# Optimization experiments

Hardware: AMD Instinct MI355X
Metric: run time of the kernel (lower is better)

Reference implementation:

```python
import jax, jax.numpy as jnp
import numpy as np

QMIN, QMAX = -128, 127  # signed int8 range


def setup_inputs() -> dict:
    key = jax.random.key(0)
    k_x, k_w, k_b = jax.random.split(key, 3)
    N, C_in, H, W = 32, 128, 56, 56
    C_out, kH, kW = 256, 3, 3
    # int8-valued tensors carried as int32 (jax-friendly); values in [-128, 127]
    x = jax.random.randint(k_x, (N, C_in, H, W), 0, 256, dtype=jnp.int32) - 128
    weight = jax.random.randint(k_w, (C_out, C_in, kH, kW), 0, 256, dtype=jnp.int32) - 128
    # int32 bias, already quantized with scale s_in * s_w
    bias = jax.random.randint(k_b, (C_out,), -(2 ** 14), 2 ** 14, dtype=jnp.int32)
    return {
        "x": x,
        "weight": weight,
        "bias": bias,
        "input_scale": jnp.float32(0.02),
        "weight_scale": jnp.float32(0.005),
        "output_scale": jnp.float32(0.05),
        "input_zero_point": jnp.int32(-5),
        "output_zero_point": jnp.int32(3),
    }


def reference(x, weight, bias, input_scale, weight_scale, output_scale,
              input_zero_point, output_zero_point):
    # Dequant-style integer conv: shift input by its zero point (weights are
    # symmetric, zero point 0), accumulate in fp32 (stands in for int32 acc).
    x_f = (x - input_zero_point).astype(jnp.float32)
    w_f = weight.astype(jnp.float32)
    acc = jax.lax.conv_general_dilated(
        x_f, w_f,
        window_strides=(1, 1),
        padding=((1, 1), (1, 1)),
        dimension_numbers=("NCHW", "OIHW", "NCHW"),
    )
    acc = acc + bias.astype(jnp.float32)[None, :, None, None]
    # Requantize: scale fusion + output zero point, round, clamp to int8.
    requant_scale = input_scale * weight_scale / output_scale
    y = acc * requant_scale + output_zero_point.astype(jnp.float32)
    y_q = jnp.clip(jnp.round(y), QMIN, QMAX).astype(jnp.int8)
    return y_q
```

## Files before the change

### kernel.cpp

```cpp
#include <hip/hip_runtime.h>
#include <stdint.h>


#define NB 32
#define CI 128
#define HH 56
#define WW 56
#define CO 256
#define SPA (HH * WW)
#define HP 58
#define WP 64
#define XP2_BYTES (NB * HP * WP * CI)
#define BP_BYTES (9 * 2 * 4 * CO * 16)
#define ABUF (6 * 8192)

typedef int v4i __attribute__((ext_vector_type(4)));

__global__ __launch_bounds__(256) void prep_kernel(
    const int* __restrict__ x, const int* __restrict__ wgt,
    const int* __restrict__ bias, const int* __restrict__ zpi,
    int8_t* __restrict__ xp2, int8_t* __restrict__ bp, int* __restrict__ BG)
{
    __shared__ int sm[1824];
    const int tid = threadIdx.x, bid = blockIdx.x;
    const int zp = *zpi;
    const int zp4 = (zp & 255) * 0x01010101;

    if (bid < HH * NB) {
        const int n = bid / HH, h = bid % HH;
        #pragma unroll
        for (int it = 0; it < 7; ++it) {
            int j = tid + it * 256;
            int ci = j / 14, w4 = j - ci * 14;
            const v4i v = *(const v4i*)(x + ((n * CI + ci) * HH + h) * WW + w4 * 4);
            sm[w4 * 130 + ci] = (v.x & 255) | ((v.y & 255) << 8) |
                                ((v.z & 255) << 16) | (v.w << 24);
        }
        __syncthreads();
        int* od = (int*)xp2 + (n * HP + h + 1) * (WP * CI / 4);
        #pragma unroll
        for (int it = 0; it < 8; ++it) {
            int j = tid + it * 256;
            int widx = j >> 5, ci4 = j & 31;
            int val = zp4;
            if (widx >= 1 && widx <= WW) {
                int w = widx - 1;
                int base = (w >> 2) * 130 + ci4 * 4;
                int sh = (w & 3) * 8;
                val = ((sm[base] >> sh) & 0xff) | (((sm[base+1] >> sh) & 0xff) << 8) |
                      (((sm[base+2] >> sh) & 0xff) << 16) | ((sm[base+3] >> sh) << 24);
            }
            od[j ^ ((widx & 7) << 2)] = val;
        }
    } else if (bid < HH * NB + 2 * NB) {
        const int z = bid - HH * NB;
        const int n = z >> 1, hidx = (z & 1) ? (HP - 1) : 0;
        int* od = (int*)xp2 + (n * HP + hidx) * (WP * CI / 4);
        #pragma unroll
        for (int it = 0; it < 8; ++it) od[tid + it * 256] = zp4;
    } else {
        const int co = bid - (HH * NB + 2 * NB);
        for (int j = tid; j < 1152; j += 256) sm[j] = wgt[co * 1152 + j];
        __syncthreads();
        for (int j = tid; j < 288; j += 256) {
            int j4 = j & 3, q = (j >> 2) & 3, c64 = (j >> 4) & 1, t = j >> 5;
            int ci = c64 * 64 + q * 16 + j4 * 4;
            int b0 = sm[(ci + 0) * 9 + t] & 255, b1 = sm[(ci + 1) * 9 + t] & 255;
            int b2 = sm[(ci + 2) * 9 + t] & 255, b3 = sm[(ci + 3) * 9 + t];
            ((int*)bp)[((t * 2 + c64) * 4 + q) * 1024 + co * 4 + j4] =
                b0 | (b1 << 8) | (b2 << 16) | (b3 << 24);
        }
        if (tid < 9) {
            int s = 0;
            for (int ci = 0; ci < CI; ++ci) s += sm[ci * 9 + tid];
            sm[1152 + tid] = s;
        }
        __syncthreads();
        if (tid == 0) {
            int s9 = 0;
            for (int t = 0; t < 9; ++t) s9 += sm[1152 + t];
            BG[co] = bias[co] - zp * s9;
        }
    }
}

__global__ __launch_bounds__(256, 1) void qconv_mfma(
    const int8_t* __restrict__ xp2, const int8_t* __restrict__ bp,
    const int* __restrict__ BG,
    const float* __restrict__ si, const float* __restrict__ sw,
    const float* __restrict__ so, const int* __restrict__ zpo,
    int* __restrict__ out)
{
    const int tid  = threadIdx.x, lane = tid & 63, wid = tid >> 6;
    const int quad = lane >> 4, lo16 = lane & 15;
    const int bid  = blockIdx.x;
    const int x    = bid & 7, r = bid >> 3;
    const int n    = x * 4 + (r & 3);
    const int co64 = (r >> 2) & 3;
    const int p    = r >> 4;
    const int mh   = wid >> 1, ch = wid & 1;
    const int cw   = co64 * 64 + ch * 32;

    __shared__ __attribute__((aligned(16))) int8_t Asm[2][ABUF];

    const int8_t* src0 = xp2 + (((size_t)n * HP + 4 * p) << 13);
    #pragma unroll
    for (int k = 0; k < 12; ++k) {
        const int u = wid + 4 * k;
        __builtin_amdgcn_global_load_lds(
            (const __attribute__((address_space(1))) void*)(src0 + (u << 10) + lane * 16),
            (__attribute__((address_space(3))) void*)(&Asm[0][u << 10]), 16, 0, 0);
    }

    v4i breg[9][2][2];
    #pragma unroll
    for (int t = 0; t < 9; ++t)
        #pragma unroll
        for (int c = 0; c < 2; ++c)
            #pragma unroll
            for (int ct = 0; ct < 2; ++ct)
                breg[t][c][ct] = *(const v4i*)(bp + (((t * 2 + c) * 4 + quad) << 12) +
                                               (cw + ct * 16 + lo16) * 16);

    int bgv[2];
    #pragma unroll
    for (int ct = 0; ct < 2; ++ct) bgv[ct] = BG[cw + ct * 16 + lo16];
    const float rs = (*si) * (*sw) / (*so);
    const float zo = (float)(*zpo);

    int rowoff[7], colp[7][3];
    #pragma unroll
    for (int mt = 0; mt < 7; ++mt) {
        const int ml = mh * 112 + mt * 16 + lo16;
        const int srow = ml / 56, scol = ml - srow * 56;
        rowoff[mt] = srow * 8192;
        #pragma unroll
        for (int dc = 0; dc < 3; ++dc) {
            const int c2 = scol + dc;
            colp[mt][dc] = (c2 * 128 + quad * 16) ^ ((c2 & 7) << 4);
        }
    }

    __syncthreads();

    #pragma unroll 1
    for (int t7 = 0; t7 < 7; ++t7) {
        const int s = p + 2 * t7;
        const int8_t* curA = Asm[t7 & 1];

        if (t7 < 6) {
            const int8_t* srcn = xp2 + (((size_t)n * HP + 4 * (s + 2)) << 13);
            int8_t* dst = (int8_t*)Asm[(t7 & 1) ^ 1];
            #pragma unroll
            for (int k = 0; k < 12; ++k) {
                const int u = wid + 4 * k;
                __builtin_amdgcn_global_load_lds(
                    (const __attribute__((address_space(1))) void*)(srcn + (u << 10) + lane * 16),
                    (__attribute__((address_space(3))) void*)(dst + (u << 10)), 16, 0, 0);
            }
        }
        __builtin_amdgcn_sched_barrier(0);

        v4i acc[7][2];
        #pragma unroll
        for (int mt = 0; mt < 7; ++mt)
            #pragma unroll
            for (int ct = 0; ct < 2; ++ct) acc[mt][ct] = (v4i){0, 0, 0, 0};

        #pragma unroll
        for (int tp = 0; tp < 9; ++tp) {
            const int dr = tp / 3, dc = tp % 3;
            #pragma unroll
            for (int mt = 0; mt < 7; ++mt) {
                const int off = rowoff[mt] + dr * 8192 + colp[mt][dc];
                v4i a0 = *(const v4i*)(curA + off);
                v4i a1 = *(const v4i*)(curA + (off ^ 64));
                acc[mt][0] = __builtin_amdgcn_mfma_i32_16x16x64_i8(a0, breg[tp][0][0], acc[mt][0], 0, 0, 0);
                acc[mt][1] = __builtin_amdgcn_mfma_i32_16x16x64_i8(a0, breg[tp][0][1], acc[mt][1], 0, 0, 0);
                acc[mt][0] = __builtin_amdgcn_mfma_i32_16x16x64_i8(a1, breg[tp][1][0], acc[mt][0], 0, 0, 0);
                acc[mt][1] = __builtin_amdgcn_mfma_i32_16x16x64_i8(a1, breg[tp][1][1], acc[mt][1], 0, 0, 0);
            }
        }

        const int m0 = s * 224 + mh * 112;
        #pragma unroll
        for (int mt = 0; mt < 7; ++mt) {
            #pragma unroll
            for (int ct = 0; ct < 2; ++ct) {
                v4i vv;
                #pragma unroll
                for (int i = 0; i < 4; ++i) {
                    float yv = rintf((float)(acc[mt][ct][i] + bgv[ct]) * rs + zo);
                    yv = fminf(fmaxf(yv, -128.f), 127.f);
                    vv[i] = (int)yv;
                }
                *(v4i*)(out + (n * CO + cw + ct * 16 + lo16) * SPA +
                        m0 + mt * 16 + quad * 4) = vv;
            }
        }

        if (t7 < 6) {
            __builtin_amdgcn_sched_barrier(0);
            asm volatile("s_waitcnt vmcnt(14)" ::: "memory");
            __builtin_amdgcn_s_barrier();
            __builtin_amdgcn_sched_barrier(0);
        }
    }
}

extern "C" void kernel_launch(void* const* d_in, const int* in_sizes, int n_in,
                              void* d_out, int out_size, void* d_ws, size_t ws_size,
                              hipStream_t stream) {
    const int*   x    = (const int*)d_in[0];
    const int*   wgt  = (const int*)d_in[1];
    const int*   bias = (const int*)d_in[2];
    const float* si   = (const float*)d_in[3];
    const float* sw   = (const float*)d_in[4];
    const float* so   = (const float*)d_in[5];
    const int*   zpi  = (const int*)d_in[6];
    const int*   zpo  = (const int*)d_in[7];
    int* out = (int*)d_out;

    int8_t* xp2 = (int8_t*)d_ws;
    int8_t* bp  = xp2 + XP2_BYTES;
    int*    bg  = (int*)(bp + BP_BYTES);

    prep_kernel<<<HH * NB + 2 * NB + CO, 256, 0, stream>>>(x, wgt, bias, zpi, xp2, bp, bg);
    qconv_mfma<<<256, 256, 0, stream>>>(xp2, bp, bg, si, sw, so, zpo, out);
}
```

Baseline: 187.4 us.

## Shrink conv tile to two output rows per step and double grid

```diff
diff --git a/kernel.cpp b/kernel.cpp
--- a/kernel.cpp
+++ b/kernel.cpp
@@ -12,7 +12,7 @@
 #define WP 64
 #define XP2_BYTES (NB * HP * WP * CI)
 #define BP_BYTES (9 * 2 * 4 * CO * 16)
-#define ABUF (6 * 8192)
+#define ABUF (4 * 8192)
 
 typedef int v4i __attribute__((ext_vector_type(4)));
 
@@ -84,7 +84,7 @@
     }
 }
 
-__global__ __launch_bounds__(256, 1) void qconv_mfma(
+__global__ __launch_bounds__(256, 2) void qconv_mfma(
     const int8_t* __restrict__ xp2, const int8_t* __restrict__ bp,
     const int* __restrict__ BG,
     const float* __restrict__ si, const float* __restrict__ sw,
@@ -97,41 +97,36 @@
     const int x    = bid & 7, r = bid >> 3;
     const int n    = x * 4 + (r & 3);
     const int co64 = (r >> 2) & 3;
-    const int p    = r >> 4;
-    const int mh   = wid >> 1, ch = wid & 1;
-    const int cw   = co64 * 64 + ch * 32;
+    const int g    = r >> 4;
+    const int cw   = co64 * 64 + wid * 16;
 
     __shared__ __attribute__((aligned(16))) int8_t Asm[2][ABUF];
 
-    const int8_t* src0 = xp2 + (((size_t)n * HP + 4 * p) << 13);
+    const int8_t* src0 = xp2 + (((size_t)n * HP + 2 * g) << 13);
     #pragma unroll
-    for (int k = 0; k < 12; ++k) {
+    for (int k = 0; k < 8; ++k) {
         const int u = wid + 4 * k;
         __builtin_amdgcn_global_load_lds(
             (const __attribute__((address_space(1))) void*)(src0 + (u << 10) + lane * 16),
             (__attribute__((address_space(3))) void*)(&Asm[0][u << 10]), 16, 0, 0);
     }
 
-    v4i breg[9][2][2];
+    v4i breg[9][2];
     #pragma unroll
     for (int t = 0; t < 9; ++t)
         #pragma unroll
         for (int c = 0; c < 2; ++c)
-            #pragma unroll
-            for (int ct = 0; ct < 2; ++ct)
-                breg[t][c][ct] = *(const v4i*)(bp + (((t * 2 + c) * 4 + quad) << 12) +
-                                               (cw + ct * 16 + lo16) * 16);
-
-    int bgv[2];
-    #pragma unroll
-    for (int ct = 0; ct < 2; ++ct) bgv[ct] = BG[cw + ct * 16 + lo16];
+            breg[t][c] = *(const v4i*)(bp + (((t * 2 + c) * 4 + quad) << 12) +
+                                       (cw + lo16) * 16);
+
+    const int bg0 = BG[cw + lo16];
     const float rs = (*si) * (*sw) / (*so);
     const float zo = (float)(*zpo);
 
     int rowoff[7], colp[7][3];
     #pragma unroll
     for (int mt = 0; mt < 7; ++mt) {
-        const int ml = mh * 112 + mt * 16 + lo16;
+        const int ml = mt * 16 + lo16;
         const int srow = ml / 56, scol = ml - srow * 56;
         rowoff[mt] = srow * 8192;
         #pragma unroll
@@ -141,18 +136,20 @@
         }
     }
 
+    int* optr = out + ((size_t)n * CO + cw + lo16) * SPA + quad * 4;
+
     __syncthreads();
 
     #pragma unroll 1
     for (int t7 = 0; t7 < 7; ++t7) {
-        const int s = p + 2 * t7;
+        const int s = g + 4 * t7;
         const int8_t* curA = Asm[t7 & 1];
 
         if (t7 < 6) {
-            const int8_t* srcn = xp2 + (((size_t)n * HP + 4 * (s + 2)) << 13);
+            const int8_t* srcn = xp2 + (((size_t)n * HP + 2 * (s + 4)) << 13);
             int8_t* dst = (int8_t*)Asm[(t7 & 1) ^ 1];
             #pragma unroll
-            for (int k = 0; k < 12; ++k) {
+            for (int k = 0; k < 8; ++k) {
                 const int u = wid + 4 * k;
                 __builtin_amdgcn_global_load_lds(
                     (const __attribute__((address_space(1))) void*)(srcn + (u << 10) + lane * 16),
@@ -161,11 +158,9 @@
         }
         __builtin_amdgcn_sched_barrier(0);
 
-        v4i acc[7][2];
-        #pragma unroll
-        for (int mt = 0; mt < 7; ++mt)
-            #pragma unroll
-            for (int ct = 0; ct < 2; ++ct) acc[mt][ct] = (v4i){0, 0, 0, 0};
+        v4i acc[7];
+        #pragma unroll
+        for (int mt = 0; mt < 7; ++mt) acc[mt] = (v4i){0, 0, 0, 0};
 
         #pragma unroll
         for (int tp = 0; tp < 9; ++tp) {
@@ -175,33 +170,27 @@
                 const int off = rowoff[mt] + dr * 8192 + colp[mt][dc];
                 v4i a0 = *(const v4i*)(curA + off);
                 v4i a1 = *(const v4i*)(curA + (off ^ 64));
-                acc[mt][0] = __builtin_amdgcn_mfma_i32_16x16x64_i8(a0, breg[tp][0][0], acc[mt][0], 0, 0, 0);
-                acc[mt][1] = __builtin_amdgcn_mfma_i32_16x16x64_i8(a0, breg[tp][0][1], acc[mt][1], 0, 0, 0);
-                acc[mt][0] = __builtin_amdgcn_mfma_i32_16x16x64_i8(a1, breg[tp][1][0], acc[mt][0], 0, 0, 0);
-                acc[mt][1] = __builtin_amdgcn_mfma_i32_16x16x64_i8(a1, breg[tp][1][1], acc[mt][1], 0, 0, 0);
-            }
-        }
-
-        const int m0 = s * 224 + mh * 112;
+                acc[mt] = __builtin_amdgcn_mfma_i32_16x16x64_i8(a0, breg[tp][0], acc[mt], 0, 0, 0);
+                acc[mt] = __builtin_amdgcn_mfma_i32_16x16x64_i8(a1, breg[tp][1], acc[mt], 0, 0, 0);
+            }
+        }
+
+        const int m0 = s * 112;
         #pragma unroll
         for (int mt = 0; mt < 7; ++mt) {
+            v4i vv;
             #pragma unroll
-            for (int ct = 0; ct < 2; ++ct) {
-                v4i vv;
-                #pragma unroll
-                for (int i = 0; i < 4; ++i) {
-                    float yv = rintf((float)(acc[mt][ct][i] + bgv[ct]) * rs + zo);
-                    yv = fminf(fmaxf(yv, -128.f), 127.f);
-                    vv[i] = (int)yv;
-                }
-                *(v4i*)(out + (n * CO + cw + ct * 16 + lo16) * SPA +
-                        m0 + mt * 16 + quad * 4) = vv;
-            }
+            for (int i = 0; i < 4; ++i) {
+                float yv = rintf((float)(acc[mt][i] + bg0) * rs + zo);
+                yv = fminf(fmaxf(yv, -128.f), 127.f);
+                vv[i] = (int)yv;
+            }
+            *(v4i*)(optr + m0 + mt * 16) = vv;
         }
 
         if (t7 < 6) {
             __builtin_amdgcn_sched_barrier(0);
-            asm volatile("s_waitcnt vmcnt(14)" ::: "memory");
+            asm volatile("s_waitcnt vmcnt(7)" ::: "memory");
             __builtin_amdgcn_s_barrier();
             __builtin_amdgcn_sched_barrier(0);
         }
@@ -226,5 +215,5 @@
     int*    bg  = (int*)(bp + BP_BYTES);
 
     prep_kernel<<<HH * NB + 2 * NB + CO, 256, 0, stream>>>(x, wgt, bias, zpi, xp2, bp, bg);
-    qconv_mfma<<<256, 256, 0, stream>>>(xp2, bp, bg, si, sw, so, zpo, out);
+    qconv_mfma<<<512, 256, 0, stream>>>(xp2, bp, bg, si, sw, so, zpo, out);
 }
```

New measurement: 180.7 us. -3.6%, faster.
